# Kernel optimization log

Hardware: AMD Instinct MI355X
Metric: run time of the kernel (lower is better)

Reference implementation:

```python
import jax, jax.numpy as jnp
import numpy as np

B, S, HID = 1, 2048, 2048
N_HEADS = 16
HEAD_DIM = HID // N_HEADS  # 128
ROPE_THETA = 10000.0
NEG_INF = -1e9


def setup_inputs() -> dict:
    key = jax.random.key(0)
    ks = jax.random.split(key, 5)
    hidden_states = jax.random.normal(ks[0], (B, S, HID), dtype=jnp.float32)
    scale = 1.0 / np.sqrt(HID)
    Wq = jax.random.normal(ks[1], (HID, HID), dtype=jnp.float32) * scale
    Wk = jax.random.normal(ks[2], (HID, HID), dtype=jnp.float32) * scale
    Wv = jax.random.normal(ks[3], (HID, HID), dtype=jnp.float32) * scale
    Wo = jax.random.normal(ks[4], (HID, HID), dtype=jnp.float32) * scale
    # additive causal mask [B, 1, S, S]: 0 on/below diag, -1e9 above
    causal = jnp.tril(jnp.ones((S, S), dtype=bool))
    attention_mask = jnp.where(causal, 0.0, NEG_INF).astype(jnp.float32)[None, None]
    attention_mask = jnp.broadcast_to(attention_mask, (B, 1, S, S))
    position_ids = jnp.broadcast_to(jnp.arange(S, dtype=jnp.int64)[None, :], (B, S))
    return {"hidden_states": hidden_states, "Wq": Wq, "Wk": Wk, "Wv": Wv,
            "Wo": Wo, "attention_mask": attention_mask, "position_ids": position_ids}


def _rotate_half(x):
    x1, x2 = jnp.split(x, 2, axis=-1)
    return jnp.concatenate((-x2, x1), axis=-1)


def _rope_cos_sin(position_ids, head_dim, dtype):
    inv_freq = 1.0 / (ROPE_THETA ** (jnp.arange(0, head_dim, 2, dtype=jnp.float32) / head_dim))
    freqs = position_ids.astype(jnp.float32)[:, :, None] * inv_freq[None, None, :]  # [b, s, d/2]
    emb = jnp.concatenate((freqs, freqs), axis=-1)  # [b, s, d]
    # unsqueeze_dim=1 -> broadcast over heads
    return jnp.cos(emb).astype(dtype)[:, None], jnp.sin(emb).astype(dtype)[:, None]


def reference(hidden_states, Wq, Wk, Wv, Wo, attention_mask, position_ids):
    b, s, h = hidden_states.shape
    d = HEAD_DIM
    def proj(W):
        return (hidden_states @ W.T).reshape(b, s, N_HEADS, d).transpose(0, 2, 1, 3)  # [b,h,s,d]
    q, k, v = proj(Wq), proj(Wk), proj(Wv)
    cos, sin = _rope_cos_sin(position_ids, d, q.dtype)
    q = q * cos + _rotate_half(q) * sin
    k = k * cos + _rotate_half(k) * sin
    scores = jnp.einsum('bhqd,bhkd->bhqk', q, k) / jnp.sqrt(jnp.float32(d))
    scores = scores + attention_mask
    probs = jax.nn.softmax(scores.astype(jnp.float32), axis=-1).astype(q.dtype)
    attn = jnp.einsum('bhqk,bhkd->bhqd', probs, v)
    out = attn.transpose(0, 2, 1, 3).reshape(b, s, h)
    return out @ Wo.T
```

## Files before the change

kernel.cpp:

```cpp
#include <hip/hip_runtime.h>

typedef _Float16 half8 __attribute__((ext_vector_type(8)));
typedef _Float16 half4 __attribute__((ext_vector_type(4)));
typedef float floatx4 __attribute__((ext_vector_type(4)));
typedef float floatx16 __attribute__((ext_vector_type(16)));

#define GLDS(gp, lp) __builtin_amdgcn_global_load_lds( \
    (const __attribute__((address_space(1))) void*)(gp), \
    (__attribute__((address_space(3))) void*)(lp), 16, 0, 0)

__global__ void cvt_f2h5(const float* __restrict__ s0, const float* __restrict__ s1,
                         const float* __restrict__ s2, const float* __restrict__ s3,
                         const float* __restrict__ s4,
                         _Float16* __restrict__ d0, _Float16* __restrict__ d1,
                         _Float16* __restrict__ d2, _Float16* __restrict__ d3,
                         _Float16* __restrict__ d4, int n8) {
  int i = blockIdx.x * 256 + threadIdx.x;
  if (i >= n8) return;
  const float* s; _Float16* d;
  switch (blockIdx.y) {
    case 0: s = s0; d = d0; break;
    case 1: s = s1; d = d1; break;
    case 2: s = s2; d = d2; break;
    case 3: s = s3; d = d3; break;
    default: s = s4; d = d4; break;
  }
  const float4* s4p = (const float4*)s;
  float4 a = s4p[2 * i], b = s4p[2 * i + 1];
  half8 h;
  h[0] = (_Float16)a.x; h[1] = (_Float16)a.y; h[2] = (_Float16)a.z; h[3] = (_Float16)a.w;
  h[4] = (_Float16)b.x; h[5] = (_Float16)b.y; h[6] = (_Float16)b.z; h[7] = (_Float16)b.w;
  *(half8*)(d + 8 * (size_t)i) = h;
}

__global__ __launch_bounds__(256) void rope_tr(_Float16* __restrict__ Q,
                                               _Float16* __restrict__ K,
                                               const _Float16* __restrict__ V,
                                               _Float16* __restrict__ Vt) {
  __shared__ _Float16 t[64][72];
  const int bid = (int)blockIdx.x;
  if (bid < 8192) {
    const int idx = bid * 256 + threadIdx.x;
    const int s = idx >> 10;
    const int hd = idx & 1023;
    const int head = hd >> 6, d = hd & 63;
    const float freq = exp2f((float)d * -0.2076205059304601f);
    const float ang = (float)s * freq;
    float sn, c;
    __sincosf(ang, &sn, &c);
    const size_t base = (size_t)s * 2048 + head * 128 + d;
    float q1 = (float)Q[base], q2 = (float)Q[base + 64];
    Q[base]      = (_Float16)(q1 * c - q2 * sn);
    Q[base + 64] = (_Float16)(q2 * c + q1 * sn);
    float k1 = (float)K[base], k2 = (float)K[base + 64];
    K[base]      = (_Float16)(k1 * c - k2 * sn);
    K[base + 64] = (_Float16)(k2 * c + k1 * sn);
  } else {
    const int b2 = bid - 8192;
    const int r0 = (b2 >> 5) * 64, c0 = (b2 & 31) * 64;
    const int tr = threadIdx.x >> 3, tc = (threadIdx.x & 7) * 8;
    #pragma unroll
    for (int p = 0; p < 2; ++p) {
      half8 v = *(const half8*)(V + (size_t)(r0 + p * 32 + tr) * 2048 + c0 + tc);
      *(half8*)&t[p * 32 + tr][tc] = v;
    }
    __syncthreads();
    #pragma unroll
    for (int p = 0; p < 2; ++p) {
      half8 v;
      #pragma unroll
      for (int j = 0; j < 8; ++j) v[j] = t[tc + j][p * 32 + tr];
      *(half8*)(Vt + (size_t)(c0 + p * 32 + tr) * 2048 + r0 + tc) = v;
    }
  }
}

__global__ __launch_bounds__(512, 1) void gemm_qkv(const _Float16* __restrict__ A,
                                                   const _Float16* __restrict__ W,
                                                   _Float16* __restrict__ Cq) {
  extern __shared__ _Float16 lds[];
  _Float16* As = lds;
  _Float16* Bs = lds + 3 * 16384;

  const int tid = threadIdx.x, lane = tid & 63, wv = tid >> 6;
  const int fr = lane & 15, fg = lane >> 4;
  const int wm = wv >> 2, wn = wv & 3;
  const int bm = blockIdx.y * 256, bn = blockIdx.x * 192;
  const _Float16* Ab = A + (size_t)bm * 2048;
  const _Float16* Bb = W + (size_t)bn * 2048;

  const int srow = lane >> 3;
  const int sgr = (lane & 7) ^ srow;

  auto stageA = [&](int t) {
    _Float16* dst = As + (t % 3) * 16384;
    const size_t coff = (size_t)t * 64 + sgr * 8;
    #pragma unroll
    for (int i = 0; i < 4; ++i) {
      const int rb = wv * 32 + i * 8;
      GLDS(Ab + (size_t)(rb + srow) * 2048 + coff, dst + rb * 64);
    }
  };
  auto stageB = [&](int t) {
    _Float16* dst = Bs + (t & 1) * 12288;
    const size_t coff = (size_t)t * 64 + sgr * 8;
    #pragma unroll
    for (int i = 0; i < 3; ++i) {
      const int rb = wv * 24 + i * 8;
      GLDS(Bb + (size_t)(rb + srow) * 2048 + coff, dst + rb * 64);
    }
  };

  const int arow = wm * 128 + fr;
  const int brow = wn * 48 + fr;
  const int sw = fr & 7;

  floatx4 acc[8][3] = {};

  stageA(0); stageB(0); stageA(1);
  asm volatile("s_waitcnt vmcnt(4)" ::: "memory");
  __builtin_amdgcn_s_barrier();

  for (int t = 0; t < 32; ++t) {
    const _Float16* Ac = As + (t % 3) * 16384;
    const _Float16* Bc = Bs + (t & 1) * 12288;
    #pragma unroll
    for (int kh = 0; kh < 2; ++kh) {
      const int sl = ((kh * 4 + fg) ^ sw) * 8;
      half8 af[8], bf[3];
      #pragma unroll
      for (int q = 0; q < 2; ++q)
        #pragma unroll
        for (int m = 0; m < 4; ++m)
          af[q * 4 + m] = *(const half8*)(Ac + (arow + q * 64 + m * 16) * 64 + sl);
      #pragma unroll
      for (int n = 0; n < 3; ++n)
        bf[n] = *(const half8*)(Bc + (brow + n * 16) * 64 + sl);
      if (kh == 0 && t + 1 < 32) stageB(t + 1);
      if (kh == 1 && t + 2 < 32) stageA(t + 2);
      __builtin_amdgcn_s_barrier();
      asm volatile("s_waitcnt lgkmcnt(0)" ::: "memory");
      __builtin_amdgcn_sched_barrier(0);
      __builtin_amdgcn_s_setprio(1);
      #pragma unroll
      for (int q = 0; q < 2; ++q)
        #pragma unroll
        for (int m = 0; m < 4; ++m)
          #pragma unroll
          for (int n = 0; n < 3; ++n)
            acc[q * 4 + m][n] =
                __builtin_amdgcn_mfma_f32_16x16x32_f16(af[q * 4 + m], bf[n],
                                                       acc[q * 4 + m][n], 0, 0, 0);
      __builtin_amdgcn_s_setprio(0);
      if (kh == 1) {
        if (t < 30)       asm volatile("s_waitcnt vmcnt(4)" ::: "memory");
        else if (t == 30) asm volatile("s_waitcnt vmcnt(0)" ::: "memory");
      }
      __builtin_amdgcn_s_barrier();
    }
  }

  #pragma unroll
  for (int m = 0; m < 8; ++m)
    #pragma unroll
    for (int n = 0; n < 3; ++n)
      #pragma unroll
      for (int i = 0; i < 4; ++i) {
        const int row = bm + wm * 128 + m * 16 + fg * 4 + i;
        const int col = bn + wn * 48 + n * 16 + fr;
        Cq[(size_t)(col >> 11) * 4194304 + (size_t)row * 2048 + (col & 2047)] =
            (_Float16)acc[m][n][i];
      }
}

template <int OUTF, int BN>
__global__ __launch_bounds__(256) void gemm_nt(const _Float16* __restrict__ A,
                                               const _Float16* __restrict__ B,
                                               _Float16* __restrict__ Ch,
                                               float* __restrict__ Cf,
                                               long long bStride, long long cStride) {
  __shared__ _Float16 As[2][128 * 32];
  __shared__ _Float16 Bs[2][BN * 32];
  const int NF = BN / 32;
  const int tid = threadIdx.x, lane = tid & 63, wv = tid >> 6;
  const int fr = lane & 15, fg = lane >> 4;
  const int bm = blockIdx.y * 128, bn = blockIdx.x * BN;
  const _Float16* Ab = A + (size_t)bm * 2048;
  const _Float16* Bb = B + (size_t)blockIdx.z * bStride + (size_t)bn * 2048;
  const int srow = lane >> 2;
  const int gsw = (lane & 3) ^ ((lane >> 3) & 3);
  const int asw = (fr >> 1) & 3;

  floatx4 acc[4][NF] = {};

  auto stage = [&](int buf, int kt) {
    #pragma unroll
    for (int r = 0; r < 2; ++r) {
      int row = r * 64 + wv * 16 + srow;
      GLDS(Ab + (size_t)row * 2048 + kt * 32 + gsw * 8, &As[buf][(r * 64 + wv * 16) * 32]);
    }
    #pragma unroll
    for (int r = 0; r < BN / 64; ++r) {
      int row = r * 64 + wv * 16 + srow;
      GLDS(Bb + (size_t)row * 2048 + kt * 32 + gsw * 8, &Bs[buf][(r * 64 + wv * 16) * 32]);
    }
  };
  const int wm = (wv >> 1) * 64, wn = (wv & 1) * (BN / 2);

  stage(0, 0);
  __syncthreads();

  #pragma unroll 2
  for (int kt = 0; kt < 64; ++kt) {
    const int cur = kt & 1;
    if (kt < 63) stage(cur ^ 1, kt + 1);
    half8 af[4], bf[NF];
    #pragma unroll
    for (int m = 0; m < 4; ++m)
      af[m] = *(const half8*)&As[cur][(wm + m * 16 + fr) * 32 + ((fg ^ asw) * 8)];
    #pragma unroll
    for (int n = 0; n < NF; ++n)
      bf[n] = *(const half8*)&Bs[cur][(wn + n * 16 + fr) * 32 + ((fg ^ asw) * 8)];
    #pragma unroll
    for (int m = 0; m < 4; ++m)
      #pragma unroll
      for (int n = 0; n < NF; ++n)
        acc[m][n] = __builtin_amdgcn_mfma_f32_16x16x32_f16(af[m], bf[n], acc[m][n], 0, 0, 0);
    __syncthreads();
  }

  #pragma unroll
  for (int m = 0; m < 4; ++m)
    #pragma unroll
    for (int n = 0; n < NF; ++n)
      #pragma unroll
      for (int i = 0; i < 4; ++i) {
        const int row = bm + wm + m * 16 + fg * 4 + i;
        const int col = bn + wn + n * 16 + fr;
        if (OUTF)
          Cf[(size_t)row * 2048 + col] = acc[m][n][i];
        else
          Ch[(size_t)blockIdx.z * cStride + (size_t)row * 2048 + col] = (_Float16)acc[m][n][i];
      }
}

__global__ __launch_bounds__(256, 2) void attn_k(const _Float16* __restrict__ Qp,
                                                 const _Float16* __restrict__ Kp,
                                                 const _Float16* __restrict__ Vt,
                                                 _Float16* __restrict__ Po,
                                                 float* __restrict__ Pr) {
  extern __shared__ _Float16 smem[];
  _Float16* Ks = smem;
  _Float16* Vs = smem + 2 * 64 * 128;
  _Float16* Pb = smem + 4 * 64 * 128;

  const int tid = threadIdx.x, lane = tid & 63, wv = tid >> 6;
  const int l31 = lane & 31, hi = lane >> 5;
  const int wq = wv >> 1, wk = wv & 1;

  const int bid = (int)blockIdx.x;
  const int head = ((bid & 7) << 1) | ((bid >> 3) & 1);
  const int L = bid >> 4;
  int g, it0, itEnd;
  if (L < 16) { g = 16 + L; it0 = 0; itEnd = 16; }
  else {
    const int j = (L - 16) >> 1;
    if ((L & 1) == 0) { g = 15 - j; it0 = 0; itEnd = g + 1; }
    else             { g = 31 - j; it0 = 16; itEnd = g + 1; }
  }
  const size_t hoff = (size_t)head * 128;
  const int qw = g * 64 + wq * 32;
  _Float16* Pw = Pb + wv * (32 * 40);

  half8 qf[8];
  const _Float16 scl = (_Float16)0.08838834764831845f;
  #pragma unroll
  for (int ks = 0; ks < 8; ++ks) {
    half8 t = *(const half8*)(Qp + (size_t)(qw + l31) * 2048 + hoff + ks * 16 + hi * 8);
    #pragma unroll
    for (int j = 0; j < 8; ++j) t[j] = (_Float16)(t[j] * scl);
    qf[ks] = t;
  }

  auto stage = [&](int buf, int it) {
    const int kv0 = it * 64;
    #pragma unroll
    for (int i = 0; i < 4; ++i) {
      const int rbase = wv * 16 + i * 4;
      const int row = rbase + (lane >> 4);
      const int gr = (lane & 15) ^ (row & 7);
      GLDS(Kp + (size_t)(kv0 + row) * 2048 + hoff + gr * 8,
           Ks + buf * 8192 + rbase * 128);
    }
    #pragma unroll
    for (int i = 0; i < 4; ++i) {
      const int rbase = wv * 32 + i * 8;
      const int row = rbase + (lane >> 3);
      const int gr = (lane & 7) ^ (row & 7);
      GLDS(Vt + (size_t)(hoff + row) * 2048 + kv0 + gr * 8,
           Vs + buf * 8192 + rbase * 64);
    }
  };

  floatx16 o[4] = {};
  float rsum = 0.0f;

  stage(0, it0);
  __syncthreads();

  int buf = 0;
  for (int it = it0; it < itEnd; ++it) {
    if (it + 1 < itEnd) stage(buf ^ 1, it + 1);
    const _Float16* Kb = Ks + buf * 8192;
    const _Float16* Vb = Vs + buf * 8192;

    const int krow = wk * 32 + l31;
    const int ksw = l31 & 7;
    floatx16 S = {};
    __builtin_amdgcn_s_setprio(1);
    #pragma unroll
    for (int ks = 0; ks < 8; ++ks) {
      half8 a = *(const half8*)(Kb + krow * 128 + (((ks * 2 + hi) ^ ksw) * 8));
      S = __builtin_amdgcn_mfma_f32_32x32x16_f16(a, qf[ks], S, 0, 0, 0);
    }
    __builtin_amdgcn_s_setprio(0);

    if (it == g) {
      const int kv0 = it * 64;
      const int qa = qw + l31;
      #pragma unroll
      for (int r = 0; r < 16; ++r) {
        const int ka = kv0 + wk * 32 + (r & 3) + 8 * (r >> 2) + 4 * hi;
        if (ka > qa) S[r] = -1e30f;
      }
    }

    #pragma unroll
    for (int r4 = 0; r4 < 4; ++r4) {
      float p0 = __expf(S[4 * r4 + 0] - 8.0f);
      float p1 = __expf(S[4 * r4 + 1] - 8.0f);
      float p2 = __expf(S[4 * r4 + 2] - 8.0f);
      float p3 = __expf(S[4 * r4 + 3] - 8.0f);
      rsum += (p0 + p1) + (p2 + p3);
      half4 pk;
      pk[0] = (_Float16)p0; pk[1] = (_Float16)p1;
      pk[2] = (_Float16)p2; pk[3] = (_Float16)p3;
      *(half4*)(Pw + l31 * 40 + r4 * 8 + hi * 4) = pk;
    }

    half8 pa0 = *(const half8*)(Pw + l31 * 40 + hi * 8);
    half8 pa1 = *(const half8*)(Pw + l31 * 40 + 16 + hi * 8);

    __builtin_amdgcn_s_setprio(1);
    #pragma unroll
    for (int dt = 0; dt < 4; ++dt) {
      const int vrow = dt * 32 + l31;
      const int vsw = vrow & 7;
      half8 b0 = *(const half8*)(Vb + vrow * 64 + (((wk * 4 + hi) ^ vsw) * 8));
      half8 b1 = *(const half8*)(Vb + vrow * 64 + (((wk * 4 + 2 + hi) ^ vsw) * 8));
      o[dt] = __builtin_amdgcn_mfma_f32_32x32x16_f16(pa0, b0, o[dt], 0, 0, 0);
      o[dt] = __builtin_amdgcn_mfma_f32_32x32x16_f16(pa1, b1, o[dt], 0, 0, 0);
    }
    __builtin_amdgcn_s_setprio(0);

    __syncthreads();
    buf ^= 1;
  }

  float* Mo = (float*)smem;
  float* Mr = (float*)(smem + 16384);
  if (wk == 1) {
    #pragma unroll
    for (int dt = 0; dt < 4; ++dt)
      #pragma unroll
      for (int r = 0; r < 16; ++r)
        Mo[((wq * 4 + dt) * 16 + r) * 64 + lane] = o[dt][r];
    Mr[wq * 64 + lane] = rsum;
  }
  __syncthreads();
  if (wk == 0) {
    rsum += Mr[wq * 64 + lane];
    float rs = rsum;
    rs += __shfl_xor(rs, 32);
    if (hi == 0) Pr[(size_t)bid * 64 + wq * 32 + l31] = rs;
    #pragma unroll
    for (int dt = 0; dt < 4; ++dt)
      #pragma unroll
      for (int r = 0; r < 16; ++r) {
        const float w = o[dt][r] + Mo[((wq * 4 + dt) * 16 + r) * 64 + lane];
        const int ql = wq * 32 + (r & 3) + 8 * (r >> 2) + 4 * hi;
        Po[(size_t)bid * 8192 + ql * 128 + dt * 32 + l31] = (_Float16)w;
      }
  }
}

__global__ __launch_bounds__(256) void attn_merge(const _Float16* __restrict__ Po,
                                                  const float* __restrict__ Pr,
                                                  _Float16* __restrict__ At) {
  const int bidx = (int)blockIdx.x;
  const int h = bidx & 15, g = bidx >> 4;
  const int hb = ((h & 1) << 3) | (h >> 1);
  const int L0 = (g >= 16) ? (g - 16) : (16 + 2 * (15 - g));
  const int U0 = L0 * 16 + hb;
  const bool two = (g >= 16);
  const int U1 = two ? ((17 + 2 * (31 - g)) * 16 + hb) : 0;
  const int t = threadIdx.x;
  const int q = t >> 2, cs = t & 3;
  const float r0 = Pr[(size_t)U0 * 64 + q];
  const float r1 = two ? Pr[(size_t)U1 * 64 + q] : 0.0f;
  const float inv = 1.0f / (r0 + r1);
  const size_t orow = (size_t)(g * 64 + q) * 2048 + h * 128;
  #pragma unroll
  for (int s = 0; s < 4; ++s) {
    const int d0 = (cs + s * 4) * 8;
    half8 a = *(const half8*)(Po + (size_t)U0 * 8192 + q * 128 + d0);
    half8 o;
    if (two) {
      half8 b = *(const half8*)(Po + (size_t)U1 * 8192 + q * 128 + d0);
      #pragma unroll
      for (int j = 0; j < 8; ++j) o[j] = (_Float16)(((float)a[j] + (float)b[j]) * inv);
    } else {
      #pragma unroll
      for (int j = 0; j < 8; ++j) o[j] = (_Float16)((float)a[j] * inv);
    }
    *(half8*)(At + orow + d0) = o;
  }
}

extern "C" void kernel_launch(void* const* d_in, const int* in_sizes, int n_in,
                              void* d_out, int out_size, void* d_ws, size_t ws_size,
                              hipStream_t stream) {
  (void)in_sizes; (void)n_in; (void)out_size; (void)ws_size;
  const float* X  = (const float*)d_in[0];
  const float* Wq = (const float*)d_in[1];
  const float* Wk = (const float*)d_in[2];
  const float* Wv = (const float*)d_in[3];
  const float* Wo = (const float*)d_in[4];
  float* out = (float*)d_out;

  const size_t SZ = 2048ull * 2048ull;
  _Float16* ws  = (_Float16*)d_ws;
  _Float16* Xh  = ws + 0 * SZ;
  _Float16* Wqh = ws + 1 * SZ;
  _Float16* Wkh = ws + 2 * SZ;
  _Float16* Wvh = ws + 3 * SZ;
  _Float16* Woh = ws + 4 * SZ;
  _Float16* Qp  = ws + 5 * SZ;
  _Float16* Kp  = ws + 6 * SZ;
  _Float16* Vp  = ws + 7 * SZ;
  _Float16* Vtg = Wqh;
  _Float16* At  = Xh;
  _Float16* Po  = Wkh;
  float*    Pr  = (float*)Vp;

  const int n8 = (int)(SZ / 8);
  dim3 blk(256);

  cvt_f2h5<<<dim3(n8 / 256, 5), blk, 0, stream>>>(X, Wq, Wk, Wv, Wo,
                                                  Xh, Wqh, Wkh, Wvh, Woh, n8);

  gemm_qkv<<<dim3(32, 8), dim3(512), 147456, stream>>>(Xh, Wqh, Qp);

  rope_tr<<<8192 + 1024, blk, 0, stream>>>(Qp, Kp, Vp, Vtg);

  const size_t attn_lds = (4 * 64 * 128 + 4 * 32 * 40) * sizeof(_Float16);
  attn_k<<<768, blk, attn_lds, stream>>>(Qp, Kp, Vtg, Po, Pr);
  attn_merge<<<512, blk, 0, stream>>>(Po, Pr, At);

  gemm_nt<1, 128><<<dim3(16, 16, 1), blk, 0, stream>>>(At, Woh, nullptr, out, 0, 0);
}
```

Baseline: 164.2 us.

## Restructure QKV GEMM inner loop and replace output GEMM with wider-K pipelined kernel

The QKV GEMM now loads both k-halves of fragments from LDS up front, issues the next global-to-LDS stages, and runs all MFMAs in one block with a single barrier per K tile instead of two. The output projection's generic gemm_nt (K-tile 32, __syncthreads) is replaced by gemm_o, which uses 64-wide K tiles with XOR swizzle, direct global-to-LDS loads, setprio around the MFMAs and two blocks per CU. The goal is fewer barriers and better overlap of memory with MFMA work. The cost is higher register pressure from holding two sets of fragments. In gemm_o every iteration also waits vmcnt(0), which may expose load latency.

```diff
diff --git a/kernel.cpp b/kernel.cpp
--- a/kernel.cpp
+++ b/kernel.cpp
@@ -124,24 +124,24 @@
   for (int t = 0; t < 32; ++t) {
     const _Float16* Ac = As + (t % 3) * 16384;
     const _Float16* Bc = Bs + (t & 1) * 12288;
+    half8 af[2][8], bf[2][3];
     #pragma unroll
     for (int kh = 0; kh < 2; ++kh) {
       const int sl = ((kh * 4 + fg) ^ sw) * 8;
-      half8 af[8], bf[3];
       #pragma unroll
       for (int q = 0; q < 2; ++q)
         #pragma unroll
         for (int m = 0; m < 4; ++m)
-          af[q * 4 + m] = *(const half8*)(Ac + (arow + q * 64 + m * 16) * 64 + sl);
+          af[kh][q * 4 + m] = *(const half8*)(Ac + (arow + q * 64 + m * 16) * 64 + sl);
       #pragma unroll
       for (int n = 0; n < 3; ++n)
-        bf[n] = *(const half8*)(Bc + (brow + n * 16) * 64 + sl);
-      if (kh == 0 && t + 1 < 32) stageB(t + 1);
-      if (kh == 1 && t + 2 < 32) stageA(t + 2);
-      __builtin_amdgcn_s_barrier();
-      asm volatile("s_waitcnt lgkmcnt(0)" ::: "memory");
-      __builtin_amdgcn_sched_barrier(0);
-      __builtin_amdgcn_s_setprio(1);
+        bf[kh][n] = *(const half8*)(Bc + (brow + n * 16) * 64 + sl);
+    }
+    if (t + 1 < 32) stageB(t + 1);
+    if (t + 2 < 32) stageA(t + 2);
+    __builtin_amdgcn_s_setprio(1);
+    #pragma unroll
+    for (int kh = 0; kh < 2; ++kh)
       #pragma unroll
       for (int q = 0; q < 2; ++q)
         #pragma unroll
@@ -149,15 +149,12 @@
           #pragma unroll
           for (int n = 0; n < 3; ++n)
             acc[q * 4 + m][n] =
-                __builtin_amdgcn_mfma_f32_16x16x32_f16(af[q * 4 + m], bf[n],
+                __builtin_amdgcn_mfma_f32_16x16x32_f16(af[kh][q * 4 + m], bf[kh][n],
                                                        acc[q * 4 + m][n], 0, 0, 0);
-      __builtin_amdgcn_s_setprio(0);
-      if (kh == 1) {
-        if (t < 30)       asm volatile("s_waitcnt vmcnt(4)" ::: "memory");
-        else if (t == 30) asm volatile("s_waitcnt vmcnt(0)" ::: "memory");
-      }
-      __builtin_amdgcn_s_barrier();
-    }
+    __builtin_amdgcn_s_setprio(0);
+    if (t < 30)       asm volatile("s_waitcnt vmcnt(4)" ::: "memory");
+    else if (t == 30) asm volatile("s_waitcnt vmcnt(0)" ::: "memory");
+    __builtin_amdgcn_s_barrier();
   }
 
   #pragma unroll
@@ -173,74 +170,87 @@
       }
 }
 
-template <int OUTF, int BN>
-__global__ __launch_bounds__(256) void gemm_nt(const _Float16* __restrict__ A,
-                                               const _Float16* __restrict__ B,
-                                               _Float16* __restrict__ Ch,
-                                               float* __restrict__ Cf,
-                                               long long bStride, long long cStride) {
-  __shared__ _Float16 As[2][128 * 32];
-  __shared__ _Float16 Bs[2][BN * 32];
-  const int NF = BN / 32;
+__global__ __launch_bounds__(256, 2) void gemm_o(const _Float16* __restrict__ A,
+                                                 const _Float16* __restrict__ B,
+                                                 float* __restrict__ out) {
+  extern __shared__ _Float16 lds[];
+  _Float16* As = lds;
+  _Float16* Bs = lds + 2 * 8192;
+
   const int tid = threadIdx.x, lane = tid & 63, wv = tid >> 6;
   const int fr = lane & 15, fg = lane >> 4;
-  const int bm = blockIdx.y * 128, bn = blockIdx.x * BN;
+  const int wm = (wv >> 1) * 64, wn = (wv & 1) * 64;
+  const int bm = blockIdx.y * 128, bn = blockIdx.x * 128;
   const _Float16* Ab = A + (size_t)bm * 2048;
-  const _Float16* Bb = B + (size_t)blockIdx.z * bStride + (size_t)bn * 2048;
-  const int srow = lane >> 2;
-  const int gsw = (lane & 3) ^ ((lane >> 3) & 3);
-  const int asw = (fr >> 1) & 3;
-
-  floatx4 acc[4][NF] = {};
-
-  auto stage = [&](int buf, int kt) {
-    #pragma unroll
-    for (int r = 0; r < 2; ++r) {
-      int row = r * 64 + wv * 16 + srow;
-      GLDS(Ab + (size_t)row * 2048 + kt * 32 + gsw * 8, &As[buf][(r * 64 + wv * 16) * 32]);
-    }
-    #pragma unroll
-    for (int r = 0; r < BN / 64; ++r) {
-      int row = r * 64 + wv * 16 + srow;
-      GLDS(Bb + (size_t)row * 2048 + kt * 32 + gsw * 8, &Bs[buf][(r * 64 + wv * 16) * 32]);
+  const _Float16* Bb = B + (size_t)bn * 2048;
+
+  const int srow = lane >> 3;
+  const int sgr = (lane & 7) ^ srow;
+  const int sw = fr & 7;
+
+  auto stageA = [&](int t) {
+    _Float16* dst = As + (t & 1) * 8192;
+    const size_t coff = (size_t)t * 64 + sgr * 8;
+    #pragma unroll
+    for (int i = 0; i < 4; ++i) {
+      const int rb = wv * 32 + i * 8;
+      GLDS(Ab + (size_t)(rb + srow) * 2048 + coff, dst + rb * 64);
     }
   };
-  const int wm = (wv >> 1) * 64, wn = (wv & 1) * (BN / 2);
-
-  stage(0, 0);
-  __syncthreads();
-
-  #pragma unroll 2
-  for (int kt = 0; kt < 64; ++kt) {
-    const int cur = kt & 1;
-    if (kt < 63) stage(cur ^ 1, kt + 1);
-    half8 af[4], bf[NF];
-    #pragma unroll
-    for (int m = 0; m < 4; ++m)
-      af[m] = *(const half8*)&As[cur][(wm + m * 16 + fr) * 32 + ((fg ^ asw) * 8)];
-    #pragma unroll
-    for (int n = 0; n < NF; ++n)
-      bf[n] = *(const half8*)&Bs[cur][(wn + n * 16 + fr) * 32 + ((fg ^ asw) * 8)];
-    #pragma unroll
-    for (int m = 0; m < 4; ++m)
-      #pragma unroll
-      for (int n = 0; n < NF; ++n)
-        acc[m][n] = __builtin_amdgcn_mfma_f32_16x16x32_f16(af[m], bf[n], acc[m][n], 0, 0, 0);
-    __syncthreads();
+  auto stageB = [&](int t) {
+    _Float16* dst = Bs + (t & 1) * 8192;
+    const size_t coff = (size_t)t * 64 + sgr * 8;
+    #pragma unroll
+    for (int i = 0; i < 4; ++i) {
+      const int rb = wv * 32 + i * 8;
+      GLDS(Bb + (size_t)(rb + srow) * 2048 + coff, dst + rb * 64);
+    }
+  };
+
+  floatx4 acc[4][4] = {};
+
+  stageA(0); stageB(0);
+  asm volatile("s_waitcnt vmcnt(0)" ::: "memory");
+  __builtin_amdgcn_s_barrier();
+
+  for (int t = 0; t < 32; ++t) {
+    const _Float16* Ac = As + (t & 1) * 8192;
+    const _Float16* Bc = Bs + (t & 1) * 8192;
+    half8 af[2][4], bf[2][4];
+    #pragma unroll
+    for (int kh = 0; kh < 2; ++kh) {
+      const int sl = ((kh * 4 + fg) ^ sw) * 8;
+      #pragma unroll
+      for (int m = 0; m < 4; ++m)
+        af[kh][m] = *(const half8*)(Ac + (wm + m * 16 + fr) * 64 + sl);
+      #pragma unroll
+      for (int n = 0; n < 4; ++n)
+        bf[kh][n] = *(const half8*)(Bc + (wn + n * 16 + fr) * 64 + sl);
+    }
+    if (t + 1 < 32) { stageA(t + 1); stageB(t + 1); }
+    __builtin_amdgcn_s_setprio(1);
+    #pragma unroll
+    for (int kh = 0; kh < 2; ++kh)
+      #pragma unroll
+      for (int m = 0; m < 4; ++m)
+        #pragma unroll
+        for (int n = 0; n < 4; ++n)
+          acc[m][n] = __builtin_amdgcn_mfma_f32_16x16x32_f16(af[kh][m], bf[kh][n],
+                                                             acc[m][n], 0, 0, 0);
+    __builtin_amdgcn_s_setprio(0);
+    asm volatile("s_waitcnt vmcnt(0)" ::: "memory");
+    __builtin_amdgcn_s_barrier();
   }
 
   #pragma unroll
   for (int m = 0; m < 4; ++m)
     #pragma unroll
-    for (int n = 0; n < NF; ++n)
+    for (int n = 0; n < 4; ++n)
       #pragma unroll
       for (int i = 0; i < 4; ++i) {
         const int row = bm + wm + m * 16 + fg * 4 + i;
         const int col = bn + wn + n * 16 + fr;
-        if (OUTF)
-          Cf[(size_t)row * 2048 + col] = acc[m][n][i];
-        else
-          Ch[(size_t)blockIdx.z * cStride + (size_t)row * 2048 + col] = (_Float16)acc[m][n][i];
+        out[(size_t)row * 2048 + col] = acc[m][n][i];
       }
 }
 
@@ -467,5 +477,5 @@
   attn_k<<<768, blk, attn_lds, stream>>>(Qp, Kp, Vtg, Po, Pr);
   attn_merge<<<512, blk, 0, stream>>>(Po, Pr, At);
 
-  gemm_nt<1, 128><<<dim3(16, 16, 1), blk, 0, stream>>>(At, Woh, nullptr, out, 0, 0);
-}
+  gemm_o<<<dim3(16, 16), blk, 65536, stream>>>(At, Woh, out);
+}
```

New measurement: 149.5 us. 1.1x faster.
